# Optimization experiments

Hardware: AMD Instinct MI355X
Metric: run time of the kernel (lower is better)

Reference implementation:

```python
import jax, jax.numpy as jnp
import numpy as np

INV_SQRT2 = 0.7071067811865476  # pywt haar: cA=(x0+x1)/sqrt2, cD=(x0-x1)/sqrt2


def haar_dwt2(x):
    # x: (..., H, W) with even H, W. Matches pywt.dwt2 (cA, (cH, cV, cD))
    # keys: cH='da' (detail along rows), cV='ad', cD='dd'.
    aw = (x[..., ::2] + x[..., 1::2]) * INV_SQRT2   # low-pass along W
    dw = (x[..., ::2] - x[..., 1::2]) * INV_SQRT2   # high-pass along W
    LL = (aw[..., ::2, :] + aw[..., 1::2, :]) * INV_SQRT2
    LH = (aw[..., ::2, :] - aw[..., 1::2, :]) * INV_SQRT2  # cH
    HL = (dw[..., ::2, :] + dw[..., 1::2, :]) * INV_SQRT2  # cV
    HH = (dw[..., ::2, :] - dw[..., 1::2, :]) * INV_SQRT2  # cD
    return LL, LH, HL, HH


def _interleave_h(e, o):
    out_shape = e.shape[:-2] + (2 * e.shape[-2], e.shape[-1])
    return jnp.stack([e, o], axis=-2).reshape(out_shape)


def _interleave_w(e, o):
    out_shape = e.shape[:-1] + (2 * e.shape[-1],)
    return jnp.stack([e, o], axis=-1).reshape(out_shape)


def haar_idwt2(LL, LH, HL, HH):
    # exact inverse of haar_dwt2 (== pywt.idwt2 for haar, even sizes)
    aw = _interleave_h((LL + LH) * INV_SQRT2, (LL - LH) * INV_SQRT2)
    dw = _interleave_h((HL + HH) * INV_SQRT2, (HL - HH) * INV_SQRT2)
    return _interleave_w((aw + dw) * INV_SQRT2, (aw - dw) * INV_SQRT2)


def conv2d(x, w, b, stride, pad):
    y = jax.lax.conv_general_dilated(
        x, w, (stride, stride), [(pad, pad), (pad, pad)],
        dimension_numbers=('NCHW', 'OIHW', 'NCHW'))
    return y + b[None, :, None, None]


def conv_transpose2d(x, w, b, stride, pad):
    # torch ConvTranspose2d weight layout: (in, out, kH, kW)
    k = w.shape[2]
    wt = jnp.flip(jnp.transpose(w, (1, 0, 2, 3)), (2, 3))  # -> (out,in,kH,kW)
    p = k - 1 - pad
    y = jax.lax.conv_general_dilated(
        x, wt, (1, 1), [(p, p), (p, p)], lhs_dilation=(stride, stride),
        dimension_numbers=('NCHW', 'OIHW', 'NCHW'))
    return y + b[None, :, None, None]


def setup_inputs() -> dict:
    key = jax.random.key(0)
    k1, k2, k3 = jax.random.split(key, 3)
    B, C, H, W = 32, 3, 512, 512
    x = jax.random.normal(k1, (B, C, H, W), dtype=jnp.float32)
    # kaiming-style init for the small 9->9 convs
    down_w = jax.random.normal(k2, (9, 9, 3, 3), dtype=jnp.float32) * np.sqrt(2.0 / (9 * 9))
    down_b = jnp.zeros((9,), dtype=jnp.float32)
    up_w = jax.random.normal(k3, (9, 9, 4, 4), dtype=jnp.float32) * np.sqrt(2.0 / (9 * 16))
    up_b = jnp.zeros((9,), dtype=jnp.float32)
    return {"x": x, "down_w": down_w, "down_b": down_b, "up_w": up_w, "up_b": up_b}


def reference(x, down_w, down_b, up_w, up_b):
    B, C, H, W = x.shape
    # ---- encode ----
    LL1, LH1, HL1, HH1 = haar_dwt2(x)      # (B,C,H/2,W/2)
    LL2, LH2, HL2, HH2 = haar_dwt2(LL1)    # (B,C,H/4,W/4)
    level2 = jnp.stack([LL2, LH2, HL2, HH2], axis=2).reshape(B, C * 4, H // 4, W // 4)
    level1 = jnp.stack([LH1, HL1, HH1], axis=2).reshape(B, C * 3, H // 2, W // 2)
    level1_down = conv2d(level1, down_w, down_b, stride=2, pad=1)  # (B,9,H/4,W/4)
    z = jnp.concatenate([level2, level1_down], axis=1)             # (B,21,H/4,W/4)
    # ---- decode ----
    l2 = z[:, :4 * C].reshape(B, C, 4, H // 4, W // 4)
    l1 = conv_transpose2d(z[:, 4 * C:], up_w, up_b, stride=2, pad=1)
    l1 = l1.reshape(B, C, 3, H // 2, W // 2)
    LL1r = haar_idwt2(l2[:, :, 0], l2[:, :, 1], l2[:, :, 2], l2[:, :, 3])
    x_rec = haar_idwt2(LL1r, l1[:, :, 0], l1[:, :, 1], l1[:, :, 2])
    return x_rec
```

## Files before the change

### kernel.cpp

```cpp
#include <hip/hip_runtime.h>


#define BB 32

__global__ __launch_bounds__(256) void k0_rearrange(
    const float* __restrict__ dw, const float* __restrict__ uw,
    float* __restrict__ wd, float* __restrict__ wu)
{
    const int t = threadIdx.x;
    for (int i = t; i < 729; i += 256) {
        const int o    = i % 9;
        const int band = (i / 9) % 3;
        const int q    = (i / 27) % 3;
        const int a    = (i / 81) % 3;
        const int ch   = i / 243;
        wd[i] = 0.5f * dw[o * 81 + (ch * 3 + band) * 9 + a * 3 + q];
    }
    for (int i = t; i < 1296; i += 256) {
        const int o = i % 9; int r = i / 9;
        const int dj = r & 1; const int di = (r >> 1) & 1; r >>= 2;
        const int ct = r & 1; const int rt = (r >> 1) & 1; const int cin = r >> 2;
        wu[i] = uw[cin * 144 + o * 16 + (3 - di - 2 * rt) * 4 + (3 - dj - 2 * ct)];
    }
}

__global__ __launch_bounds__(256) void k1_dwt_down(
    const float* __restrict__ x,
    const float* __restrict__ wd,
    const float* __restrict__ db,
    float* __restrict__ LL1,
    float* __restrict__ y)
{
    __shared__ float xs[66][68];

    const int t    = threadIdx.x;
    const int b    = blockIdx.x >> 6;
    const int tile = blockIdx.x & 63;
    const int i0   = (tile >> 3) << 4;
    const int j0   = (tile & 7) << 4;
    const int ti   = t >> 4;
    const int tj   = t & 15;
    const int I    = i0 + ti;
    const int J    = j0 + tj;

    const int gr0 = 4 * i0 - 2;
    const int gc0 = 4 * j0 - 4;

    float acc[9];
#pragma unroll
    for (int o = 0; o < 9; ++o) acc[o] = db[o];

    for (int ch = 0; ch < 3; ++ch) {
        const float* xc = x + ((size_t)b * 3 + ch) * 512 * 512;

        if (ch) __syncthreads();
        for (int idx = t; idx < 1122; idx += 256) {
            const int lr = idx / 17;
            const int f4 = idx - lr * 17;
            const int gr = gr0 + lr;
            float4 v = make_float4(0.f, 0.f, 0.f, 0.f);
            if (gr >= 0 && !(f4 == 0 && j0 == 0))
                v = *reinterpret_cast<const float4*>(xc + (size_t)gr * 512 + gc0 + 4 * f4);
            *reinterpret_cast<float4*>(&xs[lr][4 * f4]) = v;
        }
        __syncthreads();

        const float* wch = wd + ch * 243;
        float* llc = LL1 + ((size_t)b * 3 + ch) * 256 * 256;
#pragma unroll
        for (int a = 0; a < 3; ++a) {
            float2 p[2][3];
#pragma unroll
            for (int rr = 0; rr < 2; ++rr)
#pragma unroll
                for (int k = 0; k < 3; ++k)
                    p[rr][k] = *reinterpret_cast<const float2*>(
                        &xs[4 * ti + 2 * a + rr][4 * tj + 2 + 2 * k]);

            float lh[3], hl[3], hh[3], llv1, llv2;
            {
                const float s0 = p[0][0].x + p[0][0].y, d0 = p[0][0].x - p[0][0].y;
                const float s1 = p[1][0].x + p[1][0].y, d1 = p[1][0].x - p[1][0].y;
                lh[0] = s0 - s1; hl[0] = d0 + d1; hh[0] = d0 - d1;
            }
            {
                const float s0 = p[0][1].x + p[0][1].y, d0 = p[0][1].x - p[0][1].y;
                const float s1 = p[1][1].x + p[1][1].y, d1 = p[1][1].x - p[1][1].y;
                lh[1] = s0 - s1; hl[1] = d0 + d1; hh[1] = d0 - d1;
                llv1 = (s0 + s1) * 0.5f;
            }
            {
                const float s0 = p[0][2].x + p[0][2].y, d0 = p[0][2].x - p[0][2].y;
                const float s1 = p[1][2].x + p[1][2].y, d1 = p[1][2].x - p[1][2].y;
                lh[2] = s0 - s1; hl[2] = d0 + d1; hh[2] = d0 - d1;
                llv2 = (s0 + s1) * 0.5f;
            }

            if (a >= 1) {
                float2 w2; w2.x = llv1; w2.y = llv2;
                *reinterpret_cast<float2*>(llc + (size_t)(2 * I - 1 + a) * 256 + 2 * J) = w2;
            }

            const float* wg = wch + a * 81;
#pragma unroll
            for (int q = 0; q < 3; ++q) {
                const float* w0 = wg + q * 27;
#pragma unroll
                for (int o = 0; o < 9; ++o) acc[o] += lh[q] * w0[o];
#pragma unroll
                for (int o = 0; o < 9; ++o) acc[o] += hl[q] * w0[9 + o];
#pragma unroll
                for (int o = 0; o < 9; ++o) acc[o] += hh[q] * w0[18 + o];
            }
        }
    }

#pragma unroll
    for (int o = 0; o < 9; ++o)
        y[(((size_t)b * 9 + o) * 128 + I) * 128 + J] = acc[o];
}

__global__ __launch_bounds__(256, 4) void k2_up_idwt(
    const float* __restrict__ yg,
    const float* __restrict__ wu,
    const float* __restrict__ ub,
    const float* __restrict__ LL1,
    float* __restrict__ out)
{
    __shared__ float ysh[9][18][19];

    const int t    = threadIdx.x;
    const int b    = blockIdx.x >> 6;
    const int tile = blockIdx.x & 63;
    const int r0   = (tile >> 3) << 5;
    const int c0   = (tile & 7) << 5;
    const int p0   = (r0 >> 1) - 1;
    const int q0   = (c0 >> 1) - 1;

    for (int item = t; item < 9 * 324; item += 256) {
        const int cin = item / 324;
        int rem       = item - cin * 324;
        const int lp  = rem / 18;
        const int lq  = rem - lp * 18;
        const int p   = p0 + lp, q = q0 + lq;
        float v = 0.f;
        if (p >= 0 && p < 128 && q >= 0 && q < 128)
            v = yg[(((size_t)b * 9 + cin) * 128 + p) * 128 + q];
        ysh[cin][lp][lq] = v;
    }
    __syncthreads();

    const int i2 = t >> 4;
    const int j2 = t & 15;

    float acc[2][2][9];
#pragma unroll
    for (int di = 0; di < 2; ++di)
#pragma unroll
        for (int dj = 0; dj < 2; ++dj)
#pragma unroll
            for (int o = 0; o < 9; ++o) acc[di][dj][o] = ub[o];

    for (int cin = 0; cin < 9; ++cin) {
        float yv[3][3];
#pragma unroll
        for (int r = 0; r < 3; ++r)
#pragma unroll
            for (int c = 0; c < 3; ++c)
                yv[r][c] = ysh[cin][i2 + r][j2 + c];
        const float* wc = wu + cin * 144;
#pragma unroll
        for (int rt = 0; rt < 2; ++rt)
#pragma unroll
            for (int ct = 0; ct < 2; ++ct) {
                const float* wg = wc + (rt * 2 + ct) * 36;
#pragma unroll
                for (int di = 0; di < 2; ++di)
#pragma unroll
                    for (int dj = 0; dj < 2; ++dj) {
                        const float vv = yv[di + rt][dj + ct];
                        const float* w9 = wg + (di * 2 + dj) * 9;
#pragma unroll
                        for (int o = 0; o < 9; ++o)
                            acc[di][dj][o] += vv * w9[o];
                    }
            }
    }

#pragma unroll
    for (int cc = 0; cc < 3; ++cc) {
#pragma unroll
        for (int di = 0; di < 2; ++di) {
            const int I = r0 + 2 * i2 + di;
            const int J = c0 + 2 * j2;
            const float2 llv = *reinterpret_cast<const float2*>(
                LL1 + (((size_t)b * 3 + cc) * 256 + I) * 256 + J);
            float4 top, bot;
            {
                const float ll = llv.x;
                const float lh = acc[di][0][cc * 3 + 0];
                const float hl = acc[di][0][cc * 3 + 1];
                const float hh = acc[di][0][cc * 3 + 2];
                const float e0 = ll + lh, od0 = ll - lh;
                const float e1 = hl + hh, od1 = hl - hh;
                top.x = (e0 + e1) * 0.5f; top.y = (e0 - e1) * 0.5f;
                bot.x = (od0 + od1) * 0.5f; bot.y = (od0 - od1) * 0.5f;
            }
            {
                const float ll = llv.y;
                const float lh = acc[di][1][cc * 3 + 0];
                const float hl = acc[di][1][cc * 3 + 1];
                const float hh = acc[di][1][cc * 3 + 2];
                const float e0 = ll + lh, od0 = ll - lh;
                const float e1 = hl + hh, od1 = hl - hh;
                top.z = (e0 + e1) * 0.5f; top.w = (e0 - e1) * 0.5f;
                bot.z = (od0 + od1) * 0.5f; bot.w = (od0 - od1) * 0.5f;
            }
            float* op = out + (((size_t)b * 3 + cc) * 512 + 2 * I) * 512 + 2 * J;
            *reinterpret_cast<float4*>(op) = top;
            *reinterpret_cast<float4*>(op + 512) = bot;
        }
    }
}

extern "C" void kernel_launch(void* const* d_in, const int* in_sizes, int n_in,
                              void* d_out, int out_size, void* d_ws, size_t ws_size,
                              hipStream_t stream) {
    const float* x  = (const float*)d_in[0];
    const float* dw = (const float*)d_in[1];
    const float* db = (const float*)d_in[2];
    const float* uw = (const float*)d_in[3];
    const float* ub = (const float*)d_in[4];
    float* outp = (float*)d_out;

    float* wsf = (float*)d_ws;
    float* wd  = wsf;
    float* wu  = wsf + 768;
    float* LL1 = wsf + 2304;
    float* y   = LL1 + (size_t)BB * 3 * 256 * 256;

    k0_rearrange<<<dim3(1), dim3(256), 0, stream>>>(dw, uw, wd, wu);
    k1_dwt_down<<<dim3(BB * 64), dim3(256), 0, stream>>>(x, wd, db, LL1, y);
    k2_up_idwt<<<dim3(BB * 64), dim3(256), 0, stream>>>(y, wu, ub, LL1, outp);
}
```

Baseline: 102.5 us.

## Double-buffer input tiles in k1 using async global-to-LDS loads

Stages each channel's input tile into LDS with `__builtin_amdgcn_global_load_lds` direct copies, bypassing registers. It double-buffers so the next channel's load is issued while the current channel is computed. A zero pad in the workspace stands in for out-of-bounds and halo addresses. This is meant to hide global load latency behind the DWT and conv arithmetic. In exchange, LDS use per block roughly doubles, which may lower occupancy, and correctness depends on the compiler inserting the right waits before the barrier.

```diff
diff --git a/kernel.cpp b/kernel.cpp
--- a/kernel.cpp
+++ b/kernel.cpp
@@ -5,7 +5,7 @@
 
 __global__ __launch_bounds__(256) void k0_rearrange(
     const float* __restrict__ dw, const float* __restrict__ uw,
-    float* __restrict__ wd, float* __restrict__ wu)
+    float* __restrict__ wd, float* __restrict__ wu, float* __restrict__ zp)
 {
     const int t = threadIdx.x;
     for (int i = t; i < 729; i += 256) {
@@ -22,16 +22,24 @@
         const int ct = r & 1; const int rt = (r >> 1) & 1; const int cin = r >> 2;
         wu[i] = uw[cin * 144 + o * 16 + (3 - di - 2 * rt) * 4 + (3 - dj - 2 * ct)];
     }
+    if (t < 16) zp[t] = 0.f;
+}
+
+__device__ __forceinline__ void gload16(const float* gp, float* lp) {
+    __builtin_amdgcn_global_load_lds(
+        (const __attribute__((address_space(1))) void*)gp,
+        (__attribute__((address_space(3))) void*)lp, 16, 0, 0);
 }
 
 __global__ __launch_bounds__(256) void k1_dwt_down(
     const float* __restrict__ x,
     const float* __restrict__ wd,
     const float* __restrict__ db,
+    const float* __restrict__ zp,
     float* __restrict__ LL1,
     float* __restrict__ y)
 {
-    __shared__ float xs[66][68];
+    __shared__ float xs[2][4608];
 
     const int t    = threadIdx.x;
     const int b    = blockIdx.x >> 6;
@@ -42,31 +50,41 @@
     const int tj   = t & 15;
     const int I    = i0 + ti;
     const int J    = j0 + tj;
-
-    const int gr0 = 4 * i0 - 2;
-    const int gc0 = 4 * j0 - 4;
+    const int gr0  = 4 * i0 - 2;
+    const int gc0  = 4 * j0 - 4;
+    const int w    = t >> 6;
+    const int lane = t & 63;
+
+    auto stage = [&](int buf, int ch) {
+        const float* xc = x + ((size_t)b * 3 + ch) * (512 * 512);
+#pragma unroll
+        for (int n = 0; n < 5; ++n) {
+            const int s = n * 4 + w;
+            if (s >= 18) break;
+            const int idx = s * 64 + lane;
+            const int lr  = idx / 17;
+            const int f4c = idx - lr * 17;
+            const int gr  = gr0 + lr;
+            const bool ok = (idx < 1122) && (gr >= 0) && !(f4c == 0 && j0 == 0);
+            const float* gp = ok ? (xc + (size_t)gr * 512 + gc0 + 4 * f4c) : zp;
+            gload16(gp, &xs[buf][idx * 4]);
+        }
+    };
 
     float acc[9];
 #pragma unroll
     for (int o = 0; o < 9; ++o) acc[o] = db[o];
 
+    stage(0, 0);
+    __syncthreads();
+
+#pragma unroll
     for (int ch = 0; ch < 3; ++ch) {
-        const float* xc = x + ((size_t)b * 3 + ch) * 512 * 512;
-
-        if (ch) __syncthreads();
-        for (int idx = t; idx < 1122; idx += 256) {
-            const int lr = idx / 17;
-            const int f4 = idx - lr * 17;
-            const int gr = gr0 + lr;
-            float4 v = make_float4(0.f, 0.f, 0.f, 0.f);
-            if (gr >= 0 && !(f4 == 0 && j0 == 0))
-                v = *reinterpret_cast<const float4*>(xc + (size_t)gr * 512 + gc0 + 4 * f4);
-            *reinterpret_cast<float4*>(&xs[lr][4 * f4]) = v;
-        }
-        __syncthreads();
-
+        if (ch < 2) stage((ch + 1) & 1, ch + 1);
+        const int buf = ch & 1;
         const float* wch = wd + ch * 243;
-        float* llc = LL1 + ((size_t)b * 3 + ch) * 256 * 256;
+        float* llc = LL1 + ((size_t)b * 3 + ch) * (256 * 256);
+
 #pragma unroll
         for (int a = 0; a < 3; ++a) {
             float2 p[2][3];
@@ -75,7 +93,7 @@
 #pragma unroll
                 for (int k = 0; k < 3; ++k)
                     p[rr][k] = *reinterpret_cast<const float2*>(
-                        &xs[4 * ti + 2 * a + rr][4 * tj + 2 + 2 * k]);
+                        &xs[buf][(4 * ti + 2 * a + rr) * 68 + 4 * tj + 2 + 2 * k]);
 
             float lh[3], hl[3], hh[3], llv1, llv2;
             {
@@ -113,6 +131,7 @@
                 for (int o = 0; o < 9; ++o) acc[o] += hh[q] * w0[18 + o];
             }
         }
+        if (ch < 2) __syncthreads();
     }
 
 #pragma unroll
@@ -236,10 +255,11 @@
     float* wsf = (float*)d_ws;
     float* wd  = wsf;
     float* wu  = wsf + 768;
+    float* zp  = wsf + 2240;
     float* LL1 = wsf + 2304;
     float* y   = LL1 + (size_t)BB * 3 * 256 * 256;
 
-    k0_rearrange<<<dim3(1), dim3(256), 0, stream>>>(dw, uw, wd, wu);
-    k1_dwt_down<<<dim3(BB * 64), dim3(256), 0, stream>>>(x, wd, db, LL1, y);
+    k0_rearrange<<<dim3(1), dim3(256), 0, stream>>>(dw, uw, wd, wu, zp);
+    k1_dwt_down<<<dim3(BB * 64), dim3(256), 0, stream>>>(x, wd, db, zp, LL1, y);
     k2_up_idwt<<<dim3(BB * 64), dim3(256), 0, stream>>>(y, wu, ub, LL1, outp);
 }
```

After: 91.19 us. 1.12x faster.
